# Kernel optimization log

Hardware: AMD Instinct MI355X
Metric: run time of the kernel (lower is better)

The kernel has to match this reference:

```python
import jax, jax.numpy as jnp
import numpy as np

FIX_SIGMA = (1.0, 2.0, 4.0, 8.0, 16.0)


def setup_inputs() -> dict:
    key = jax.random.key(0)
    k1, k2 = jax.random.split(key)
    B, C, D = 512, 32, 512
    source = jax.random.normal(k1, (B, C, D), dtype=jnp.float32)
    target = jax.random.normal(k2, (B, C, D), dtype=jnp.float32)
    return {"source": source, "target": target}


def _mmd(source, target):
    B = source.shape[0]
    total = jnp.concatenate([source, target], axis=0)  # [N, C, D], N = 2B
    # Pairwise per-channel squared L2 distance via norm expansion
    # (mathematically identical to ((x_i - x_j)**2).sum(-1), no [N,N,C,D] intermediate)
    sq = jnp.sum(total * total, axis=-1)  # [N, C]
    cross = jnp.einsum("icd,jcd->ijc", total, total)  # [N, N, C]
    L2 = sq[:, None, :] + sq[None, :, :] - 2.0 * cross  # [N, N, C]
    kernels = sum(jnp.exp(-L2 / sigma) for sigma in FIX_SIGMA)  # [N, N, C]
    XX = kernels[:B, :B, :]
    YY = kernels[B:, B:, :]
    XY = kernels[:B, B:, :]
    YX = kernels[B:, :B, :]
    loss_1 = XX + YY - XY - YX  # [B, B, C]
    # mean over dim0, mean over dim0 again (i.e. both batch dims), sum over channels
    return jnp.sum(jnp.mean(loss_1, axis=(0, 1)))


def reference(source, target):
    return _mmd(source, target)
```

## Files before the change

### kernel.cpp

```cpp
#include <hip/hip_runtime.h>

namespace {

constexpr int kC = 32;
constexpr int kD = 512;
constexpr int kB = 512;
constexpr int kN = 1024;
constexpr int kCD = kC * kD;
constexpr int BM = 128;
constexpr int BKt = 32;
constexpr int KT = kD / BKt;
constexpr int TILES = kN / BM;
constexpr int NP = TILES * (TILES + 1) / 2;

typedef float f32x4 __attribute__((ext_vector_type(4)));
typedef short s16x8 __attribute__((ext_vector_type(8)));

__device__ inline unsigned int pack_bf16(float a, float b) {
  unsigned int ua = __float_as_uint(a);
  unsigned int ub = __float_as_uint(b);
  ua += 0x7fffu + ((ua >> 16) & 1u);
  ub += 0x7fffu + ((ub >> 16) & 1u);
  return (ua >> 16) | (ub & 0xffff0000u);
}

__global__ void prep_kernel(const float* __restrict__ src,
                            const float* __restrict__ tgt,
                            float* __restrict__ sq,
                            unsigned int* __restrict__ tot,
                            float* __restrict__ out) {
  if (blockIdx.x == 0 && threadIdx.x == 0) *out = 0.f;
  int gw = (blockIdx.x * blockDim.x + threadIdx.x) >> 6;
  int lane = threadIdx.x & 63;
  int i = gw >> 5;
  int c = gw & 31;
  const float* p = (i < kB ? src + (size_t)i * kCD
                           : tgt + (size_t)(i - kB) * kCD) + c * kD;
  f32x4 v0 = *(const f32x4*)(p + lane * 8);
  f32x4 v1 = *(const f32x4*)(p + lane * 8 + 4);

  uint4 w = make_uint4(pack_bf16(v0.x, v0.y), pack_bf16(v0.z, v0.w),
                       pack_bf16(v1.x, v1.y), pack_bf16(v1.z, v1.w));
  *(uint4*)(tot + (size_t)(c * kN + i) * (kD / 2) + lane * 4) = w;

  float s = v0.x * v0.x + v0.y * v0.y + v0.z * v0.z + v0.w * v0.w
          + v1.x * v1.x + v1.y * v1.y + v1.z * v1.z + v1.w * v1.w;
#pragma unroll
  for (int o = 32; o > 0; o >>= 1) s += __shfl_down(s, o);
  if (lane == 0) sq[c * kN + i] = s;
}

__launch_bounds__(128, 2)
__global__ void mmd_kernel(const unsigned short* __restrict__ tot,
                           const float* __restrict__ sq,
                           float* __restrict__ out) {
  const int b = blockIdx.x;
  const int c = b & 31;
  int p = b >> 5;
  int ti = 0;
  while (p >= TILES - ti) { p -= TILES - ti; ++ti; }
  const int tj = ti + p;

  __shared__ __align__(16) unsigned short lA[2][BM * BKt];
  __shared__ __align__(16) unsigned short lB[2][BM * BKt];
  __shared__ float wsum[2];

  const int t = threadIdx.x;
  const int lane = t & 63;
  const int wid = t >> 6;

  const unsigned short* gA = tot + (size_t)(c * kN + ti * BM) * kD;
  const unsigned short* gB = tot + (size_t)(c * kN + tj * BM) * kD;

  const int srow = ((lane >> 3) << 1) + ((lane >> 2) & 1);
  const int scch = (lane & 3) ^ ((lane >> 3) & 3);

  auto STAGE = [&](int buf, int ks) {
#pragma unroll
    for (int q = 0; q < 4; ++q) {
      int seg = wid * 4 + q;
      int r = 16 * seg + srow;
      size_t off = (size_t)r * kD + ks * BKt + scch * 8;
      __builtin_amdgcn_global_load_lds(
          (const __attribute__((address_space(1))) unsigned int*)(gA + off),
          (__attribute__((address_space(3))) unsigned int*)&lA[buf][seg * 512],
          16, 0, 0);
      __builtin_amdgcn_global_load_lds(
          (const __attribute__((address_space(1))) unsigned int*)(gB + off),
          (__attribute__((address_space(3))) unsigned int*)&lB[buf][seg * 512],
          16, 0, 0);
    }
  };

  const int l15 = lane & 15;
  const int s4 = lane >> 4;
  const int laneoff = ((l15 >> 1) << 7) + ((l15 & 1) << 6) +
                      ((s4 ^ ((l15 >> 1) & 3)) << 4);

  f32x4 acc[8][4] = {};

  STAGE(0, 0);

#pragma unroll
  for (int ks = 0; ks < KT; ++ks) {
    asm volatile("s_waitcnt vmcnt(0)" ::: "memory");
    __builtin_amdgcn_sched_barrier(0);
    __builtin_amdgcn_s_barrier();

    const int buf = ks & 1;
    if (ks + 1 < KT) STAGE(buf ^ 1, ks + 1);

    const char* Abase = (const char*)lA[buf] + laneoff;
    const char* Bbase = (const char*)lB[buf] + wid * 4096 + laneoff;
    s16x8 aF[8], bF[4];
#pragma unroll
    for (int m = 0; m < 8; ++m) aF[m] = *(const s16x8*)(Abase + m * 1024);
#pragma unroll
    for (int n = 0; n < 4; ++n) bF[n] = *(const s16x8*)(Bbase + n * 1024);

    __builtin_amdgcn_s_setprio(1);
#pragma unroll
    for (int m = 0; m < 8; ++m)
#pragma unroll
      for (int n = 0; n < 4; ++n)
        acc[m][n] = __builtin_amdgcn_mfma_f32_16x16x32_bf16(
            aF[m], bF[n], acc[m][n], 0, 0, 0);
    __builtin_amdgcn_s_setprio(0);
  }

  const float sgn = ((ti < TILES / 2) == (tj < TILES / 2)) ? 1.f : -1.f;
  const float scale = sgn * ((ti == tj) ? 1.f : 2.f) / 262144.f;
  const float* sqA = sq + c * kN + ti * BM;
  const float* sqB = sq + c * kN + tj * BM + wid * 64;

  float local = 0.f;
#pragma unroll
  for (int m = 0; m < 8; ++m) {
    float sqa_r[4];
#pragma unroll
    for (int rI = 0; rI < 4; ++rI)
      sqa_r[rI] = sqA[m * 16 + s4 * 4 + rI];
#pragma unroll
    for (int n = 0; n < 4; ++n) {
      float sqb_ = sqB[n * 16 + l15];
#pragma unroll
      for (int rI = 0; rI < 4; ++rI) {
        float L2 = sqa_r[rI] + sqb_ - 2.f * acc[m][n][rI];
        float tt = __expf(L2 * -0.0625f);
        float t2 = tt * tt, t4 = t2 * t2, t8 = t4 * t4;
        local += tt + t2 + t4 + t8 + t8 * t8;
      }
    }
  }
  local *= scale;

#pragma unroll
  for (int o = 32; o > 0; o >>= 1) local += __shfl_down(local, o);
  if (lane == 0) wsum[wid] = local;
  __syncthreads();
  if (t == 0) atomicAdd(out, wsum[0] + wsum[1]);
}

}

extern "C" void kernel_launch(void* const* d_in, const int* in_sizes, int n_in,
                              void* d_out, int out_size, void* d_ws,
                              size_t ws_size, hipStream_t stream) {
  const float* src = (const float*)d_in[0];
  const float* tgt = (const float*)d_in[1];
  float* out = (float*)d_out;

  float* sq = (float*)d_ws;
  unsigned int* tot = (unsigned int*)((char*)d_ws + (size_t)kC * kN * 4);

  {
    int blocks = (kN * kC) / 4;
    prep_kernel<<<blocks, 256, 0, stream>>>(src, tgt, sq, tot, out);
  }
  {
    int blocks = NP * kC;
    mmd_kernel<<<blocks, 128, 0, stream>>>((const unsigned short*)tot, sq, out);
  }
}
```

Baseline: 62.28 us.

## Switch Gram computation to FP8 MFMA with pre-tiled layout and triple buffering

Quantizes inputs to FP8 e4m3 in the prep kernel instead of bf16 and writes them in an MFMA-fragment-friendly tiled layout through shared-memory staging. The main kernel uses fp8 16x16x32 MFMA on 4 waves with a 2x2 warp tiling, and triple-buffered LDS loads two stages ahead. It also forces zero distance on the diagonal so self-similarity is not hurt by quantization error. This halves operand bandwidth and raises MFMA throughput, at a large cost in precision for the cross terms, which may break accuracy tolerance.

```diff
diff --git a/kernel.cpp b/kernel.cpp
--- a/kernel.cpp
+++ b/kernel.cpp
@@ -8,50 +8,77 @@
 constexpr int kN = 1024;
 constexpr int kCD = kC * kD;
 constexpr int BM = 128;
-constexpr int BKt = 32;
-constexpr int KT = kD / BKt;
+constexpr int KT = kD / 32;
 constexpr int TILES = kN / BM;
 constexpr int NP = TILES * (TILES + 1) / 2;
 
 typedef float f32x4 __attribute__((ext_vector_type(4)));
-typedef short s16x8 __attribute__((ext_vector_type(8)));
-
-__device__ inline unsigned int pack_bf16(float a, float b) {
-  unsigned int ua = __float_as_uint(a);
-  unsigned int ub = __float_as_uint(b);
-  ua += 0x7fffu + ((ua >> 16) & 1u);
-  ub += 0x7fffu + ((ub >> 16) & 1u);
-  return (ua >> 16) | (ub & 0xffff0000u);
+
+__device__ inline unsigned int f32_to_e4m3(float x) {
+  unsigned int u = __float_as_uint(x);
+  unsigned int s = (u >> 24) & 0x80u;
+  unsigned int ax = u & 0x7fffffffu;
+  if (ax < 0x3c800000u) {
+    unsigned int m = (unsigned int)(__uint_as_float(ax) * 512.0f + 0.5f);
+    return s | (m > 7u ? 8u : m);
+  }
+  if (ax > 0x43e00000u) return s | 0x7eu;
+  unsigned int r = ax + 0x7ffffu + ((ax >> 20) & 1u);
+  unsigned int e = (r >> 23) - 120u;
+  return s | (e << 3) | ((r >> 20) & 7u);
 }
 
 __global__ void prep_kernel(const float* __restrict__ src,
                             const float* __restrict__ tgt,
                             float* __restrict__ sq,
-                            unsigned int* __restrict__ tot,
+                            unsigned char* __restrict__ tot,
                             float* __restrict__ out) {
   if (blockIdx.x == 0 && threadIdx.x == 0) *out = 0.f;
-  int gw = (blockIdx.x * blockDim.x + threadIdx.x) >> 6;
-  int lane = threadIdx.x & 63;
-  int i = gw >> 5;
-  int c = gw & 31;
+  const int seg = blockIdx.x >> 5;
+  const int c = blockIdx.x & 31;
+  const int t = threadIdx.x;
+  const int slot = t & 15;
+  const int ks = t >> 4;
+
+  const int i = seg * 16 + slot;
   const float* p = (i < kB ? src + (size_t)i * kCD
-                           : tgt + (size_t)(i - kB) * kCD) + c * kD;
-  f32x4 v0 = *(const f32x4*)(p + lane * 8);
-  f32x4 v1 = *(const f32x4*)(p + lane * 8 + 4);
-
-  uint4 w = make_uint4(pack_bf16(v0.x, v0.y), pack_bf16(v0.z, v0.w),
-                       pack_bf16(v1.x, v1.y), pack_bf16(v1.z, v1.w));
-  *(uint4*)(tot + (size_t)(c * kN + i) * (kD / 2) + lane * 4) = w;
-
-  float s = v0.x * v0.x + v0.y * v0.y + v0.z * v0.z + v0.w * v0.w
+                           : tgt + (size_t)(i - kB) * kCD) + c * kD + ks * 32;
+
+  __shared__ unsigned int stg[2048];
+  __shared__ float sqp[256];
+
+  float part = 0.f;
+#pragma unroll
+  for (int q = 0; q < 4; ++q) {
+    f32x4 v0 = *(const f32x4*)(p + q * 8);
+    f32x4 v1 = *(const f32x4*)(p + q * 8 + 4);
+    part += v0.x * v0.x + v0.y * v0.y + v0.z * v0.z + v0.w * v0.w
           + v1.x * v1.x + v1.y * v1.y + v1.z * v1.z + v1.w * v1.w;
-#pragma unroll
-  for (int o = 32; o > 0; o >>= 1) s += __shfl_down(s, o);
-  if (lane == 0) sq[c * kN + i] = s;
-}
-
-__launch_bounds__(128, 2)
-__global__ void mmd_kernel(const unsigned short* __restrict__ tot,
+    unsigned int lo = f32_to_e4m3(v0.x) | (f32_to_e4m3(v0.y) << 8) |
+                      (f32_to_e4m3(v0.z) << 16) | (f32_to_e4m3(v0.w) << 24);
+    unsigned int hi = f32_to_e4m3(v1.x) | (f32_to_e4m3(v1.y) << 8) |
+                      (f32_to_e4m3(v1.z) << 16) | (f32_to_e4m3(v1.w) << 24);
+    int idx = ks * 128 + q * 32 + slot * 2;
+    stg[idx] = lo;
+    stg[idx + 1] = hi;
+  }
+  sqp[t] = part;
+  __syncthreads();
+
+  unsigned char* gout = tot + (size_t)(c * 64 + seg) * 8192;
+  ((uint4*)gout)[t * 2]     = ((const uint4*)stg)[t * 2];
+  ((uint4*)gout)[t * 2 + 1] = ((const uint4*)stg)[t * 2 + 1];
+
+  if (t < 16) {
+    float s = 0.f;
+#pragma unroll
+    for (int j = 0; j < 16; ++j) s += sqp[t + 16 * j];
+    sq[c * kN + seg * 16 + t] = s;
+  }
+}
+
+__launch_bounds__(256, 4)
+__global__ void mmd_kernel(const unsigned char* __restrict__ tot,
                            const float* __restrict__ sq,
                            float* __restrict__ out) {
   const int b = blockIdx.x;
@@ -61,81 +88,78 @@
   while (p >= TILES - ti) { p -= TILES - ti; ++ti; }
   const int tj = ti + p;
 
-  __shared__ __align__(16) unsigned short lA[2][BM * BKt];
-  __shared__ __align__(16) unsigned short lB[2][BM * BKt];
-  __shared__ float wsum[2];
+  __shared__ __align__(16) unsigned char lA[3][4096];
+  __shared__ __align__(16) unsigned char lB[3][4096];
+  __shared__ float wsum[4];
 
   const int t = threadIdx.x;
   const int lane = t & 63;
   const int wid = t >> 6;
-
-  const unsigned short* gA = tot + (size_t)(c * kN + ti * BM) * kD;
-  const unsigned short* gB = tot + (size_t)(c * kN + tj * BM) * kD;
-
-  const int srow = ((lane >> 3) << 1) + ((lane >> 2) & 1);
-  const int scch = (lane & 3) ^ ((lane >> 3) & 3);
+  const int wr = wid >> 1;
+  const int wcn = wid & 1;
+
+  const size_t blkA = (size_t)(c * 64 + ti * 8 + 2 * wid + (lane >> 5));
+  const size_t blkB = (size_t)(c * 64 + tj * 8 + 2 * wid + (lane >> 5));
+  const int loff16 = (lane & 31) * 16;
 
   auto STAGE = [&](int buf, int ks) {
-#pragma unroll
-    for (int q = 0; q < 4; ++q) {
-      int seg = wid * 4 + q;
-      int r = 16 * seg + srow;
-      size_t off = (size_t)r * kD + ks * BKt + scch * 8;
-      __builtin_amdgcn_global_load_lds(
-          (const __attribute__((address_space(1))) unsigned int*)(gA + off),
-          (__attribute__((address_space(3))) unsigned int*)&lA[buf][seg * 512],
-          16, 0, 0);
-      __builtin_amdgcn_global_load_lds(
-          (const __attribute__((address_space(1))) unsigned int*)(gB + off),
-          (__attribute__((address_space(3))) unsigned int*)&lB[buf][seg * 512],
-          16, 0, 0);
-    }
+    const unsigned char* sa = tot + (blkA * 16 + ks) * 512 + loff16;
+    const unsigned char* sb = tot + (blkB * 16 + ks) * 512 + loff16;
+    __builtin_amdgcn_global_load_lds(
+        (const __attribute__((address_space(1))) unsigned int*)sa,
+        (__attribute__((address_space(3))) unsigned int*)&lA[buf][wid * 1024],
+        16, 0, 0);
+    __builtin_amdgcn_global_load_lds(
+        (const __attribute__((address_space(1))) unsigned int*)sb,
+        (__attribute__((address_space(3))) unsigned int*)&lB[buf][wid * 1024],
+        16, 0, 0);
   };
 
-  const int l15 = lane & 15;
-  const int s4 = lane >> 4;
-  const int laneoff = ((l15 >> 1) << 7) + ((l15 & 1) << 6) +
-                      ((s4 ^ ((l15 >> 1) & 3)) << 4);
-
-  f32x4 acc[8][4] = {};
+  const int fo = ((lane >> 4) << 4) + (lane & 15);
+
+  f32x4 acc[4][4] = {};
 
   STAGE(0, 0);
+  STAGE(1, 1);
 
 #pragma unroll
   for (int ks = 0; ks < KT; ++ks) {
-    asm volatile("s_waitcnt vmcnt(0)" ::: "memory");
+    if (ks + 1 < KT) asm volatile("s_waitcnt vmcnt(2)" ::: "memory");
+    else             asm volatile("s_waitcnt vmcnt(0)" ::: "memory");
     __builtin_amdgcn_sched_barrier(0);
     __builtin_amdgcn_s_barrier();
 
-    const int buf = ks & 1;
-    if (ks + 1 < KT) STAGE(buf ^ 1, ks + 1);
-
-    const char* Abase = (const char*)lA[buf] + laneoff;
-    const char* Bbase = (const char*)lB[buf] + wid * 4096 + laneoff;
-    s16x8 aF[8], bF[4];
-#pragma unroll
-    for (int m = 0; m < 8; ++m) aF[m] = *(const s16x8*)(Abase + m * 1024);
-#pragma unroll
-    for (int n = 0; n < 4; ++n) bF[n] = *(const s16x8*)(Bbase + n * 1024);
+    const int buf = ks % 3;
+    const long* A64 = (const long*)lA[buf];
+    const long* B64 = (const long*)lB[buf];
+    long aF[4], bF[4];
+#pragma unroll
+    for (int m = 0; m < 4; ++m) aF[m] = A64[(4 * wr + m) * 64 + fo];
+#pragma unroll
+    for (int n = 0; n < 4; ++n) bF[n] = B64[(4 * wcn + n) * 64 + fo];
+
+    if (ks + 2 < KT) STAGE((ks + 2) % 3, ks + 2);
 
     __builtin_amdgcn_s_setprio(1);
 #pragma unroll
-    for (int m = 0; m < 8; ++m)
+    for (int m = 0; m < 4; ++m)
 #pragma unroll
       for (int n = 0; n < 4; ++n)
-        acc[m][n] = __builtin_amdgcn_mfma_f32_16x16x32_bf16(
+        acc[m][n] = __builtin_amdgcn_mfma_f32_16x16x32_fp8_fp8(
             aF[m], bF[n], acc[m][n], 0, 0, 0);
     __builtin_amdgcn_s_setprio(0);
   }
 
   const float sgn = ((ti < TILES / 2) == (tj < TILES / 2)) ? 1.f : -1.f;
-  const float scale = sgn * ((ti == tj) ? 1.f : 2.f) / 262144.f;
-  const float* sqA = sq + c * kN + ti * BM;
-  const float* sqB = sq + c * kN + tj * BM + wid * 64;
+  const bool diag = (ti == tj);
+  const float scale = sgn * (diag ? 1.f : 2.f) / 262144.f;
+  const float* sqA = sq + c * kN + ti * BM + wr * 64;
+  const float* sqB = sq + c * kN + tj * BM + wcn * 64;
+  const int s4 = lane >> 4, l15 = lane & 15;
 
   float local = 0.f;
 #pragma unroll
-  for (int m = 0; m < 8; ++m) {
+  for (int m = 0; m < 4; ++m) {
     float sqa_r[4];
 #pragma unroll
     for (int rI = 0; rI < 4; ++rI)
@@ -146,6 +170,9 @@
 #pragma unroll
       for (int rI = 0; rI < 4; ++rI) {
         float L2 = sqa_r[rI] + sqb_ - 2.f * acc[m][n][rI];
+        if (diag && (wr * 64 + m * 16 + s4 * 4 + rI) ==
+                    (wcn * 64 + n * 16 + l15))
+          L2 = 0.f;
         float tt = __expf(L2 * -0.0625f);
         float t2 = tt * tt, t4 = t2 * t2, t8 = t4 * t4;
         local += tt + t2 + t4 + t8 + t8 * t8;
@@ -158,7 +185,8 @@
   for (int o = 32; o > 0; o >>= 1) local += __shfl_down(local, o);
   if (lane == 0) wsum[wid] = local;
   __syncthreads();
-  if (t == 0) atomicAdd(out, wsum[0] + wsum[1]);
+  if (t == 0)
+    atomicAdd(out, wsum[0] + wsum[1] + wsum[2] + wsum[3]);
 }
 
 }
@@ -171,14 +199,14 @@
   float* out = (float*)d_out;
 
   float* sq = (float*)d_ws;
-  unsigned int* tot = (unsigned int*)((char*)d_ws + (size_t)kC * kN * 4);
+  unsigned char* tot = (unsigned char*)d_ws + (size_t)kC * kN * 4;
 
   {
-    int blocks = (kN * kC) / 4;
+    int blocks = 64 * kC;
     prep_kernel<<<blocks, 256, 0, stream>>>(src, tgt, sq, tot, out);
   }
   {
     int blocks = NP * kC;
-    mmd_kernel<<<blocks, 128, 0, stream>>>((const unsigned short*)tot, sq, out);
-  }
-}
+    mmd_kernel<<<blocks, 256, 0, stream>>>(tot, sq, out);
+  }
+}
```

Result: no change. 62.13 us (-0.2%).
